# Kernel tuning notes

Measured on AMD Instinct MI355X. Metric: run time of the kernel, lower is better.

Reference implementation:

```python
import jax, jax.numpy as jnp
import numpy as np

DIM = 192
HEADS = 6
EPS = 1e-12  # torch F.normalize eps


def dwconv(x, w, b):
    # x: (B,C,H,W), w: (C,1,3,3) depthwise kernel, b: (C,)
    y = jax.lax.conv_general_dilated(
        x, w, window_strides=(1, 1), padding='SAME',
        feature_group_count=x.shape[1],
        dimension_numbers=('NCHW', 'OIHW', 'NCHW'))
    return y + b[None, :, None, None]


def setup_inputs() -> dict:
    key = jax.random.key(0)
    ks = jax.random.split(key, 9)
    x = jax.random.normal(ks[0], (8, DIM, 128, 128), dtype=jnp.float32)
    s = 1.0 / np.sqrt(9.0)
    wq = jax.random.normal(ks[1], (DIM, 1, 3, 3), dtype=jnp.float32) * s
    bq = jax.random.normal(ks[2], (DIM,), dtype=jnp.float32) * 0.01
    wk = jax.random.normal(ks[3], (DIM, 1, 3, 3), dtype=jnp.float32) * s
    bk = jax.random.normal(ks[4], (DIM,), dtype=jnp.float32) * 0.01
    wv = jax.random.normal(ks[5], (DIM, 1, 3, 3), dtype=jnp.float32) * s
    bv = jax.random.normal(ks[6], (DIM,), dtype=jnp.float32) * 0.01
    wp = jax.random.normal(ks[7], (DIM, DIM), dtype=jnp.float32) / np.sqrt(DIM)
    bp = jax.random.normal(ks[8], (DIM,), dtype=jnp.float32) * 0.01
    return {'x': x, 'wq': wq, 'bq': bq, 'wk': wk, 'bk': bk,
            'wv': wv, 'bv': bv, 'wp': wp, 'bp': bp}


def reference(x, wq, bq, wk, bk, wv, bv, wp, bp):
    b, c, h, w = x.shape
    hw = h * w
    ch = c // HEADS  # channels per head
    q = dwconv(x, wq, bq).reshape(b, HEADS, ch, hw)
    k = dwconv(x, wk, bk).reshape(b, HEADS, ch, hw)
    v = dwconv(x, wv, bv).reshape(b, HEADS, ch, hw)
    # L2 normalize along spatial dim (torch F.normalize semantics)
    q = q / jnp.maximum(jnp.linalg.norm(q, axis=-1, keepdims=True), EPS)
    k = k / jnp.maximum(jnp.linalg.norm(k, axis=-1, keepdims=True), EPS)
    attn = jnp.einsum('bhcn,bhdn->bhcd', q, k)  # (b,head,ch,ch)
    attn = jax.nn.softmax(attn, axis=-1)
    out = jnp.einsum('bhcd,bhdn->bhcn', attn, v)
    out = out.reshape(b, c, h, w)
    # 1x1 projection
    out = jnp.einsum('oc,bchw->bohw', wp, out) + bp[None, :, None, None]
    return out
```

## Files before the change

kernel.cpp:

```cpp
#include <hip/hip_runtime.h>

#define NB 8
#define NC 192
#define HEADS 6
#define CHH 32
#define IMH 128
#define IMW 128
#define NHW (IMH*IMW)
#define EPSN 1e-12f
#define NBCHW (NB*NC*NHW)

typedef __attribute__((ext_vector_type(8))) short short8_t;
typedef __attribute__((ext_vector_type(4))) float floatx4;
typedef unsigned short ushort_t;

#define MFMA_B16(a,b,c) __builtin_amdgcn_mfma_f32_16x16x32_bf16(a,b,c,0,0,0)

__device__ __forceinline__ ushort_t f2bf(float v){
  union { float f; unsigned u; } x; x.f = v;
  unsigned r = x.u + 0x7fffu + ((x.u >> 16) & 1u);
  return (ushort_t)(r >> 16);
}
__device__ __forceinline__ float bf2f(ushort_t h){
  union { unsigned u; float f; } x; x.u = ((unsigned)h) << 16;
  return x.f;
}
__device__ __forceinline__ void split8(const float* f, short8_t& hi, short8_t& lo){
#pragma unroll
  for (int i = 0; i < 8; ++i) {
    ushort_t h = f2bf(f[i]);
    hi[i] = (short)h;
    lo[i] = (short)f2bf(f[i] - bf2f(h));
  }
}

__global__ __launch_bounds__(256) void k1_conv_gram(
    const float* __restrict__ x,
    const float* __restrict__ wq, const float* __restrict__ bq,
    const float* __restrict__ wk, const float* __restrict__ bk,
    const float* __restrict__ wv, const float* __restrict__ bv,
    ushort_t* __restrict__ vhi, ushort_t* __restrict__ vlo,
    float* __restrict__ qn, float* __restrict__ kn,
    float* __restrict__ attn)
{
  __shared__ float qls[CHH*132];
  __shared__ float kls[CHH*132];
  __shared__ float vls[CHH*132];
  const int t  = threadIdx.x;
  const int b  = blockIdx.x / HEADS;
  const int h  = blockIdx.x % HEADS;
  const int r0 = blockIdx.y * 8;
  const int c   = t >> 3;
  const int s   = t & 7;
  const int px0 = s * 16;
  const int cg  = h*CHH + c;
  const float* xplane = x + (size_t)(b*NC + cg)*NHW;

  float wqr[9], wkr[9], wvr[9];
#pragma unroll
  for (int m = 0; m < 9; ++m) {
    wqr[m] = wq[cg*9+m]; wkr[m] = wk[cg*9+m]; wvr[m] = wv[cg*9+m];
  }
  const float bqv = bq[cg], bkv = bk[cg], bvv = bv[cg];

  const int lane  = t & 63;
  const int wid   = t >> 6;
  const int pw    = wid * 32;
  const int gsel  = lane >> 4;
  const int arow0 = (lane & 15)*132 + pw + gsel*8;

  floatx4 acc[2][2];
#pragma unroll
  for (int mt = 0; mt < 2; ++mt)
#pragma unroll
    for (int nt = 0; nt < 2; ++nt) acc[mt][nt] = (floatx4){0.f,0.f,0.f,0.f};
  float qnacc = 0.f, knacc = 0.f;

  for (int r = r0; r < r0 + 8; ++r) {
    float xr[3][18];
#pragma unroll
    for (int dr = 0; dr < 3; ++dr) {
      const int rr = r - 1 + dr;
      if (rr >= 0 && rr < IMH) {
        const float* rp = xplane + rr*IMW;
        xr[dr][0] = (px0 > 0) ? rp[px0-1] : 0.f;
#pragma unroll
        for (int q4 = 0; q4 < 4; ++q4) {
          const float4 fv = *(const float4*)(rp + px0 + q4*4);
          xr[dr][1+q4*4+0] = fv.x; xr[dr][1+q4*4+1] = fv.y;
          xr[dr][1+q4*4+2] = fv.z; xr[dr][1+q4*4+3] = fv.w;
        }
        xr[dr][17] = (px0 + 16 < IMW) ? rp[px0+16] : 0.f;
      } else {
#pragma unroll
        for (int j = 0; j < 18; ++j) xr[dr][j] = 0.f;
      }
    }
    float qst[4], kst[4], vst[4];
#pragma unroll
    for (int p = 0; p < 16; ++p) {
      float qa = bqv, ka = bkv, va = bvv;
#pragma unroll
      for (int dy = 0; dy < 3; ++dy)
#pragma unroll
        for (int dx = 0; dx < 3; ++dx) {
          const float xv = xr[dy][p+dx];
          qa = fmaf(wqr[dy*3+dx], xv, qa);
          ka = fmaf(wkr[dy*3+dx], xv, ka);
          va = fmaf(wvr[dy*3+dx], xv, va);
        }
      qnacc = fmaf(qa, qa, qnacc);
      knacc = fmaf(ka, ka, knacc);
      qst[p&3] = qa; kst[p&3] = ka; vst[p&3] = va;
      if ((p&3) == 3) {
        *(float4*)&qls[c*132 + px0 + p - 3] = make_float4(qst[0],qst[1],qst[2],qst[3]);
        *(float4*)&kls[c*132 + px0 + p - 3] = make_float4(kst[0],kst[1],kst[2],kst[3]);
        *(float4*)&vls[c*132 + px0 + p - 3] = make_float4(vst[0],vst[1],vst[2],vst[3]);
      }
    }
    __syncthreads();

    {
      short8_t qh[2], qlo[2], kh[2], klo[2];
#pragma unroll
      for (int mt = 0; mt < 2; ++mt) {
        float fa[8];
        const float* pq = &qls[mt*16*132 + arow0];
        float4 a0 = *(const float4*)pq; float4 a1 = *(const float4*)(pq+4);
        fa[0]=a0.x; fa[1]=a0.y; fa[2]=a0.z; fa[3]=a0.w;
        fa[4]=a1.x; fa[5]=a1.y; fa[6]=a1.z; fa[7]=a1.w;
        split8(fa, qh[mt], qlo[mt]);
        const float* pk = &kls[mt*16*132 + arow0];
        float4 b0 = *(const float4*)pk; float4 b1 = *(const float4*)(pk+4);
        fa[0]=b0.x; fa[1]=b0.y; fa[2]=b0.z; fa[3]=b0.w;
        fa[4]=b1.x; fa[5]=b1.y; fa[6]=b1.z; fa[7]=b1.w;
        split8(fa, kh[mt], klo[mt]);
      }
#pragma unroll
      for (int mt = 0; mt < 2; ++mt)
#pragma unroll
        for (int nt = 0; nt < 2; ++nt) {
          acc[mt][nt] = MFMA_B16(qh[mt],  kh[nt],  acc[mt][nt]);
          acc[mt][nt] = MFMA_B16(qh[mt],  klo[nt], acc[mt][nt]);
          acc[mt][nt] = MFMA_B16(qlo[mt], kh[nt],  acc[mt][nt]);
        }
    }

#pragma unroll
    for (int cc2 = 0; cc2 < 2; ++cc2) {
      const int id  = cc2*256 + t;
      const int oct = id & 3;
      const int px  = id >> 2;
      float f[8];
#pragma unroll
      for (int i = 0; i < 8; ++i) f[i] = vls[(oct*8+i)*132 + px];
      unsigned uh[4], ul[4];
#pragma unroll
      for (int j = 0; j < 4; ++j) {
        ushort_t h0 = f2bf(f[2*j]),   h1 = f2bf(f[2*j+1]);
        ushort_t l0 = f2bf(f[2*j]   - bf2f(h0));
        ushort_t l1 = f2bf(f[2*j+1] - bf2f(h1));
        uh[j] = (unsigned)h0 | ((unsigned)h1 << 16);
        ul[j] = (unsigned)l0 | ((unsigned)l1 << 16);
      }
      const size_t tile  = ((size_t)b*1024 + (size_t)r*8 + (px>>4))*6 + h;
      const size_t gbase = (tile*64 + (size_t)(oct*16 + (px&15))) * 8;
      *(uint4*)(vhi + gbase) = make_uint4(uh[0],uh[1],uh[2],uh[3]);
      *(uint4*)(vlo + gbase) = make_uint4(ul[0],ul[1],ul[2],ul[3]);
    }
    __syncthreads();
  }

  qnacc += __shfl_xor(qnacc, 1); qnacc += __shfl_xor(qnacc, 2); qnacc += __shfl_xor(qnacc, 4);
  knacc += __shfl_xor(knacc, 1); knacc += __shfl_xor(knacc, 2); knacc += __shfl_xor(knacc, 4);
  if (s == 0) {
    atomicAdd(qn + b*NC + cg, qnacc);
    atomicAdd(kn + b*NC + cg, knacc);
  }

  float* red = qls;
#pragma unroll
  for (int mt = 0; mt < 2; ++mt)
#pragma unroll
    for (int nt = 0; nt < 2; ++nt)
#pragma unroll
      for (int rg = 0; rg < 4; ++rg)
        red[wid*1024 + (mt*2+nt)*256 + lane*4 + rg] = acc[mt][nt][rg];
  __syncthreads();
  float* abuf = attn + (b*HEADS + h)*(CHH*CHH);
#pragma unroll
  for (int e = 0; e < 4; ++e) {
    const int idx = e*256 + t;
    const float sum = red[idx] + red[1024+idx] + red[2048+idx] + red[3072+idx];
    const int tile = idx >> 8;
    const int ln   = (idx >> 2) & 63;
    const int rg   = idx & 3;
    const int cc   = (tile>>1)*16 + (ln>>4)*4 + rg;
    const int dd   = (tile&1)*16 + (ln & 15);
    atomicAdd(abuf + cc*CHH + dd, sum);
  }
}

__global__ __launch_bounds__(256) void k2_softmax_M(
    const float* __restrict__ wp,
    const float* __restrict__ qn, const float* __restrict__ kn,
    const float* __restrict__ attn,
    short8_t* __restrict__ mhi, short8_t* __restrict__ mlo)
{
  __shared__ float a[CHH][CHH+1];
  __shared__ float qs[CHH], ks_[CHH];
  const int t = threadIdx.x;
  const int b = blockIdx.x / HEADS;
  const int h = blockIdx.x % HEADS;
  const float* raw = attn + (b*HEADS + h)*(CHH*CHH);
  if (t < CHH) {
    qs[t]  = fmaxf(sqrtf(qn[b*NC + h*CHH + t]), EPSN);
    ks_[t] = fmaxf(sqrtf(kn[b*NC + h*CHH + t]), EPSN);
  }
  __syncthreads();
#pragma unroll
  for (int rep = 0; rep < 4; ++rep) {
    const int idx = rep*256 + t;
    const int cc = idx >> 5, dd = idx & 31;
    a[cc][dd] = raw[idx] / (qs[cc] * ks_[dd]);
  }
  __syncthreads();
  if (t < CHH) {
    float m = -1e30f;
    for (int d = 0; d < CHH; ++d) m = fmaxf(m, a[t][d]);
    float sum = 0.f;
    for (int d = 0; d < CHH; ++d) { const float e = expf(a[t][d] - m); a[t][d] = e; sum += e; }
    const float inv = 1.f / sum;
    for (int d = 0; d < CHH; ++d) a[t][d] *= inv;
  }
  __syncthreads();
#pragma unroll
  for (int rep = 0; rep < 3; ++rep) {
    const int slot = rep*256 + t;
    const int o = slot >> 2;
    const int g = slot & 3;
    float m[8];
#pragma unroll
    for (int i = 0; i < 8; ++i) m[i] = 0.f;
    for (int cp = 0; cp < CHH; ++cp) {
      const float w = wp[o*NC + h*CHH + cp];
#pragma unroll
      for (int i = 0; i < 8; ++i) m[i] = fmaf(w, a[cp][g*8+i], m[i]);
    }
    short8_t hi, lo;
    split8(m, hi, lo);
    const size_t mi = (((size_t)b*12 + (o>>4))*6 + h)*64 + g*16 + (o&15);
    mhi[mi] = hi; mlo[mi] = lo;
  }
}

__global__ __launch_bounds__(256) void k3_gemm(
    const short8_t* __restrict__ vhi, const short8_t* __restrict__ vlo,
    const short8_t* __restrict__ mhi, const short8_t* __restrict__ mlo,
    const float* __restrict__ bp, float* __restrict__ out)
{
  const int t    = threadIdx.x;
  const int b    = blockIdx.y;
  const int lane = t & 63;
  const int w    = t >> 6;
  const int whw  = w & 1;
  const int wo   = w >> 1;
  const int ht0  = blockIdx.x*8 + whw*4;
  const int ot0  = wo*6;
  const int gsel = lane >> 4, l15 = lane & 15;

  floatx4 acc[6][4];
#pragma unroll
  for (int ot = 0; ot < 6; ++ot)
#pragma unroll
    for (int nt = 0; nt < 4; ++nt) acc[ot][nt] = (floatx4){0.f,0.f,0.f,0.f};

  const size_t vbase = ((size_t)b*1024 + ht0)*6;
  const size_t mbase = ((size_t)b*12 + ot0)*6;
#pragma unroll 2
  for (int ks = 0; ks < 6; ++ks) {
    short8_t bh[4], bl[4];
#pragma unroll
    for (int nt = 0; nt < 4; ++nt) {
      const size_t vi = (vbase + (size_t)nt*6 + ks)*64 + lane;
      bh[nt] = vhi[vi]; bl[nt] = vlo[vi];
    }
#pragma unroll
    for (int ot = 0; ot < 6; ++ot) {
      const size_t mi = (mbase + (size_t)ot*6 + ks)*64 + lane;
      const short8_t ah = mhi[mi];
      const short8_t al = mlo[mi];
#pragma unroll
      for (int nt = 0; nt < 4; ++nt) {
        acc[ot][nt] = MFMA_B16(ah, bh[nt], acc[ot][nt]);
        acc[ot][nt] = MFMA_B16(ah, bl[nt], acc[ot][nt]);
        acc[ot][nt] = MFMA_B16(al, bh[nt], acc[ot][nt]);
      }
    }
  }
#pragma unroll
  for (int ot = 0; ot < 6; ++ot) {
#pragma unroll
    for (int rg = 0; rg < 4; ++rg) {
      const int o = (ot0 + ot)*16 + gsel*4 + rg;
      const float bpv = bp[o];
#pragma unroll
      for (int nt = 0; nt < 4; ++nt) {
        const int hw = (ht0 + nt)*16 + l15;
        out[((size_t)(b*NC + o))*NHW + hw] = acc[ot][nt][rg] + bpv;
      }
    }
  }
}

extern "C" void kernel_launch(void* const* d_in, const int* in_sizes, int n_in,
                              void* d_out, int out_size, void* d_ws, size_t ws_size,
                              hipStream_t stream)
{
  const float* x  = (const float*)d_in[0];
  const float* wq = (const float*)d_in[1];
  const float* bq = (const float*)d_in[2];
  const float* wk = (const float*)d_in[3];
  const float* bk = (const float*)d_in[4];
  const float* wv = (const float*)d_in[5];
  const float* bv = (const float*)d_in[6];
  const float* wp = (const float*)d_in[7];
  const float* bp = (const float*)d_in[8];
  float* out = (float*)d_out;

  ushort_t* vhi = (ushort_t*)d_ws;
  ushort_t* vlo = vhi + (size_t)NBCHW;
  float* fbase  = (float*)(vlo + (size_t)NBCHW);
  float* qn     = fbase;
  float* kn     = qn + NB*NC;
  float* attn   = kn + NB*NC;
  short8_t* mhi = (short8_t*)(attn + NB*HEADS*CHH*CHH);
  short8_t* mlo = mhi + (size_t)NB*12*6*64;

  hipMemsetAsync(fbase, 0,
                 (size_t)(2*NB*NC + NB*HEADS*CHH*CHH)*sizeof(float), stream);

  k1_conv_gram<<<dim3(NB*HEADS, 16), 256, 0, stream>>>(
      x, wq, bq, wk, bk, wv, bv, vhi, vlo, qn, kn, attn);
  k2_softmax_M<<<NB*HEADS, 256, 0, stream>>>(wp, qn, kn, attn, mhi, mlo);
  k3_gemm<<<dim3(NHW/128, NB), 256, 0, stream>>>(
      (const short8_t*)vhi, (const short8_t*)vlo, mhi, mlo, bp, out);
}
```

Measured before the change: 282.2 us.

## Switch split-precision MFMA from bf16 to fp16 and store V as single fp16

Replaces the bf16 hi/lo splits with fp16 splits. V is now written as a single fp16 plane instead of hi+lo bf16, which halves V workspace traffic and cuts the final GEMM from three MFMAs per tile to two. The conv/gram kernel is restructured to process each row in two 64-pixel halves. It packs Q/K hi/lo and V as fp16 in a smaller shared buffer, with launch bounds set to target 4 blocks per SM. The risk is reduced accuracy on V from a single fp16 rounding, plus fp16 range limits on unnormalized activations.

After: 537.6 us. 90.5% more time.

```diff
diff --git a/kernel.cpp b/kernel.cpp
--- a/kernel.cpp
+++ b/kernel.cpp
@@ -10,50 +10,48 @@
 #define EPSN 1e-12f
 #define NBCHW (NB*NC*NHW)
 
-typedef __attribute__((ext_vector_type(8))) short short8_t;
+typedef _Float16 half8 __attribute__((ext_vector_type(8)));
 typedef __attribute__((ext_vector_type(4))) float floatx4;
 typedef unsigned short ushort_t;
 
-#define MFMA_B16(a,b,c) __builtin_amdgcn_mfma_f32_16x16x32_bf16(a,b,c,0,0,0)
-
-__device__ __forceinline__ ushort_t f2bf(float v){
-  union { float f; unsigned u; } x; x.f = v;
-  unsigned r = x.u + 0x7fffu + ((x.u >> 16) & 1u);
-  return (ushort_t)(r >> 16);
-}
-__device__ __forceinline__ float bf2f(ushort_t h){
-  union { unsigned u; float f; } x; x.u = ((unsigned)h) << 16;
-  return x.f;
-}
-__device__ __forceinline__ void split8(const float* f, short8_t& hi, short8_t& lo){
-#pragma unroll
-  for (int i = 0; i < 8; ++i) {
-    ushort_t h = f2bf(f[i]);
-    hi[i] = (short)h;
-    lo[i] = (short)f2bf(f[i] - bf2f(h));
-  }
-}
-
-__global__ __launch_bounds__(256) void k1_conv_gram(
+#define MFMA_F16(a,b,c) __builtin_amdgcn_mfma_f32_16x16x32_f16(a,b,c,0,0,0)
+
+__device__ __forceinline__ unsigned pk2(float a, float b){
+  union { _Float16 h[2]; unsigned u; } x;
+  x.h[0] = (_Float16)a; x.h[1] = (_Float16)b; return x.u;
+}
+__device__ __forceinline__ void pksplit(float a, float b, unsigned& hi, unsigned& lo){
+  _Float16 ha = (_Float16)a, hb = (_Float16)b;
+  float ra = a - (float)ha, rb = b - (float)hb;
+  union { _Float16 h[2]; unsigned u; } x;
+  x.h[0] = ha; x.h[1] = hb; hi = x.u;
+  x.h[0] = (_Float16)ra; x.h[1] = (_Float16)rb; lo = x.u;
+}
+
+#define PLN 1152
+#define QH 0
+#define QL (1*PLN)
+#define KH (2*PLN)
+#define KL (3*PLN)
+#define VV (4*PLN)
+
+__global__ __launch_bounds__(256, 4) void k1_conv_gram(
     const float* __restrict__ x,
     const float* __restrict__ wq, const float* __restrict__ bq,
     const float* __restrict__ wk, const float* __restrict__ bk,
     const float* __restrict__ wv, const float* __restrict__ bv,
-    ushort_t* __restrict__ vhi, ushort_t* __restrict__ vlo,
+    ushort_t* __restrict__ vout,
     float* __restrict__ qn, float* __restrict__ kn,
     float* __restrict__ attn)
 {
-  __shared__ float qls[CHH*132];
-  __shared__ float kls[CHH*132];
-  __shared__ float vls[CHH*132];
+  __shared__ unsigned sm[5*PLN];
   const int t  = threadIdx.x;
   const int b  = blockIdx.x / HEADS;
   const int h  = blockIdx.x % HEADS;
   const int r0 = blockIdx.y * 8;
-  const int c   = t >> 3;
-  const int s   = t & 7;
-  const int px0 = s * 16;
-  const int cg  = h*CHH + c;
+  const int c  = t >> 3;
+  const int s  = t & 7;
+  const int cg = h*CHH + c;
   const float* xplane = x + (size_t)(b*NC + cg)*NHW;
 
   float wqr[9], wkr[9], wvr[9];
@@ -63,11 +61,10 @@
   }
   const float bqv = bq[cg], bkv = bk[cg], bvv = bv[cg];
 
-  const int lane  = t & 63;
-  const int wid   = t >> 6;
-  const int pw    = wid * 32;
-  const int gsel  = lane >> 4;
-  const int arow0 = (lane & 15)*132 + pw + gsel*8;
+  const int lane = t & 63;
+  const int wid  = t >> 6;
+  const int gsel = lane >> 4, l15 = lane & 15;
+  const int oct  = wid;
 
   floatx4 acc[2][2];
 #pragma unroll
@@ -77,98 +74,94 @@
   float qnacc = 0.f, knacc = 0.f;
 
   for (int r = r0; r < r0 + 8; ++r) {
-    float xr[3][18];
-#pragma unroll
-    for (int dr = 0; dr < 3; ++dr) {
-      const int rr = r - 1 + dr;
-      if (rr >= 0 && rr < IMH) {
-        const float* rp = xplane + rr*IMW;
-        xr[dr][0] = (px0 > 0) ? rp[px0-1] : 0.f;
-#pragma unroll
-        for (int q4 = 0; q4 < 4; ++q4) {
-          const float4 fv = *(const float4*)(rp + px0 + q4*4);
-          xr[dr][1+q4*4+0] = fv.x; xr[dr][1+q4*4+1] = fv.y;
-          xr[dr][1+q4*4+2] = fv.z; xr[dr][1+q4*4+3] = fv.w;
+#pragma unroll
+    for (int half = 0; half < 2; ++half) {
+      const int px0 = half*64 + s*8;
+      float xr[3][10];
+#pragma unroll
+      for (int dr = 0; dr < 3; ++dr) {
+        const int rr = r - 1 + dr;
+        if (rr >= 0 && rr < IMH) {
+          const float* rp = xplane + rr*IMW;
+          xr[dr][0] = (px0 > 0) ? rp[px0-1] : 0.f;
+          const float4 f0 = *(const float4*)(rp + px0);
+          const float4 f1 = *(const float4*)(rp + px0 + 4);
+          xr[dr][1]=f0.x; xr[dr][2]=f0.y; xr[dr][3]=f0.z; xr[dr][4]=f0.w;
+          xr[dr][5]=f1.x; xr[dr][6]=f1.y; xr[dr][7]=f1.z; xr[dr][8]=f1.w;
+          xr[dr][9] = (px0 + 8 < IMW) ? rp[px0+8] : 0.f;
+        } else {
+#pragma unroll
+          for (int j = 0; j < 10; ++j) xr[dr][j] = 0.f;
         }
-        xr[dr][17] = (px0 + 16 < IMW) ? rp[px0+16] : 0.f;
-      } else {
-#pragma unroll
-        for (int j = 0; j < 18; ++j) xr[dr][j] = 0.f;
-      }
-    }
-    float qst[4], kst[4], vst[4];
-#pragma unroll
-    for (int p = 0; p < 16; ++p) {
-      float qa = bqv, ka = bkv, va = bvv;
-#pragma unroll
-      for (int dy = 0; dy < 3; ++dy)
-#pragma unroll
-        for (int dx = 0; dx < 3; ++dx) {
-          const float xv = xr[dy][p+dx];
-          qa = fmaf(wqr[dy*3+dx], xv, qa);
-          ka = fmaf(wkr[dy*3+dx], xv, ka);
-          va = fmaf(wvr[dy*3+dx], xv, va);
+      }
+      float qv[8], kv[8], vv8[8];
+#pragma unroll
+      for (int p = 0; p < 8; ++p) {
+        float qa = bqv, ka = bkv, va = bvv;
+#pragma unroll
+        for (int dy = 0; dy < 3; ++dy)
+#pragma unroll
+          for (int dx = 0; dx < 3; ++dx) {
+            const float xv = xr[dy][p+dx];
+            qa = fmaf(wqr[dy*3+dx], xv, qa);
+            ka = fmaf(wkr[dy*3+dx], xv, ka);
+            va = fmaf(wvr[dy*3+dx], xv, va);
+          }
+        qnacc = fmaf(qa, qa, qnacc);
+        knacc = fmaf(ka, ka, knacc);
+        qv[p] = qa; kv[p] = ka; vv8[p] = va;
+      }
+      unsigned qhp[4], qlp[4], khp[4], klp[4], vvp[4];
+#pragma unroll
+      for (int j = 0; j < 4; ++j) {
+        pksplit(qv[2*j], qv[2*j+1], qhp[j], qlp[j]);
+        pksplit(kv[2*j], kv[2*j+1], khp[j], klp[j]);
+        vvp[j] = pk2(vv8[2*j], vv8[2*j+1]);
+      }
+      const int wb = c*36 + s*4;
+      *(uint4*)&sm[QH + wb] = make_uint4(qhp[0],qhp[1],qhp[2],qhp[3]);
+      *(uint4*)&sm[QL + wb] = make_uint4(qlp[0],qlp[1],qlp[2],qlp[3]);
+      *(uint4*)&sm[KH + wb] = make_uint4(khp[0],khp[1],khp[2],khp[3]);
+      *(uint4*)&sm[KL + wb] = make_uint4(klp[0],klp[1],klp[2],klp[3]);
+      *(uint4*)&sm[VV + wb] = make_uint4(vvp[0],vvp[1],vvp[2],vvp[3]);
+      __syncthreads();
+
+      {
+        const int px = lane;
+        const int ph = px >> 1, sel = (px & 1) * 16;
+        unsigned w4[4];
+#pragma unroll
+        for (int i2 = 0; i2 < 4; ++i2) {
+          const unsigned ua = sm[VV + (oct*8 + 2*i2    )*36 + ph];
+          const unsigned ub = sm[VV + (oct*8 + 2*i2 + 1)*36 + ph];
+          w4[i2] = ((ua >> sel) & 0xffffu) | (((ub >> sel) & 0xffffu) << 16);
         }
-      qnacc = fmaf(qa, qa, qnacc);
-      knacc = fmaf(ka, ka, knacc);
-      qst[p&3] = qa; kst[p&3] = ka; vst[p&3] = va;
-      if ((p&3) == 3) {
-        *(float4*)&qls[c*132 + px0 + p - 3] = make_float4(qst[0],qst[1],qst[2],qst[3]);
-        *(float4*)&kls[c*132 + px0 + p - 3] = make_float4(kst[0],kst[1],kst[2],kst[3]);
-        *(float4*)&vls[c*132 + px0 + p - 3] = make_float4(vst[0],vst[1],vst[2],vst[3]);
-      }
-    }
-    __syncthreads();
-
-    {
-      short8_t qh[2], qlo[2], kh[2], klo[2];
-#pragma unroll
-      for (int mt = 0; mt < 2; ++mt) {
-        float fa[8];
-        const float* pq = &qls[mt*16*132 + arow0];
-        float4 a0 = *(const float4*)pq; float4 a1 = *(const float4*)(pq+4);
-        fa[0]=a0.x; fa[1]=a0.y; fa[2]=a0.z; fa[3]=a0.w;
-        fa[4]=a1.x; fa[5]=a1.y; fa[6]=a1.z; fa[7]=a1.w;
-        split8(fa, qh[mt], qlo[mt]);
-        const float* pk = &kls[mt*16*132 + arow0];
-        float4 b0 = *(const float4*)pk; float4 b1 = *(const float4*)(pk+4);
-        fa[0]=b0.x; fa[1]=b0.y; fa[2]=b0.z; fa[3]=b0.w;
-        fa[4]=b1.x; fa[5]=b1.y; fa[6]=b1.z; fa[7]=b1.w;
-        split8(fa, kh[mt], klo[mt]);
-      }
-#pragma unroll
-      for (int mt = 0; mt < 2; ++mt)
-#pragma unroll
-        for (int nt = 0; nt < 2; ++nt) {
-          acc[mt][nt] = MFMA_B16(qh[mt],  kh[nt],  acc[mt][nt]);
-          acc[mt][nt] = MFMA_B16(qh[mt],  klo[nt], acc[mt][nt]);
-          acc[mt][nt] = MFMA_B16(qlo[mt], kh[nt],  acc[mt][nt]);
+        const size_t tile = ((size_t)b*1024 + (size_t)r*8 + half*4 + (px>>4))*6 + h;
+        ushort_t* dst = vout + tile*512 + (size_t)(oct*16 + (px&15))*8;
+        *(uint4*)dst = make_uint4(w4[0],w4[1],w4[2],w4[3]);
+      }
+      if ((wid >> 1) == half) {
+        const int col = (wid & 1)*16 + gsel*4;
+        half8 aqh[2], aql[2], akh[2], akl[2];
+#pragma unroll
+        for (int mt = 0; mt < 2; ++mt) {
+          const int row = (mt*16 + l15)*36 + col;
+          aqh[mt] = *(const half8*)&sm[QH + row];
+          aql[mt] = *(const half8*)&sm[QL + row];
+          akh[mt] = *(const half8*)&sm[KH + row];
+          akl[mt] = *(const half8*)&sm[KL + row];
         }
-    }
-
-#pragma unroll
-    for (int cc2 = 0; cc2 < 2; ++cc2) {
-      const int id  = cc2*256 + t;
-      const int oct = id & 3;
-      const int px  = id >> 2;
-      float f[8];
-#pragma unroll
-      for (int i = 0; i < 8; ++i) f[i] = vls[(oct*8+i)*132 + px];
-      unsigned uh[4], ul[4];
-#pragma unroll
-      for (int j = 0; j < 4; ++j) {
-        ushort_t h0 = f2bf(f[2*j]),   h1 = f2bf(f[2*j+1]);
-        ushort_t l0 = f2bf(f[2*j]   - bf2f(h0));
-        ushort_t l1 = f2bf(f[2*j+1] - bf2f(h1));
-        uh[j] = (unsigned)h0 | ((unsigned)h1 << 16);
-        ul[j] = (unsigned)l0 | ((unsigned)l1 << 16);
-      }
-      const size_t tile  = ((size_t)b*1024 + (size_t)r*8 + (px>>4))*6 + h;
-      const size_t gbase = (tile*64 + (size_t)(oct*16 + (px&15))) * 8;
-      *(uint4*)(vhi + gbase) = make_uint4(uh[0],uh[1],uh[2],uh[3]);
-      *(uint4*)(vlo + gbase) = make_uint4(ul[0],ul[1],ul[2],ul[3]);
-    }
-    __syncthreads();
+#pragma unroll
+        for (int mt = 0; mt < 2; ++mt)
+#pragma unroll
+          for (int nt = 0; nt < 2; ++nt) {
+            acc[mt][nt] = MFMA_F16(aqh[mt], akh[nt], acc[mt][nt]);
+            acc[mt][nt] = MFMA_F16(aqh[mt], akl[nt], acc[mt][nt]);
+            acc[mt][nt] = MFMA_F16(aql[mt], akh[nt], acc[mt][nt]);
+          }
+      }
+      __syncthreads();
+    }
   }
 
   qnacc += __shfl_xor(qnacc, 1); qnacc += __shfl_xor(qnacc, 2); qnacc += __shfl_xor(qnacc, 4);
@@ -178,7 +171,7 @@
     atomicAdd(kn + b*NC + cg, knacc);
   }
 
-  float* red = qls;
+  float* red = (float*)sm;
 #pragma unroll
   for (int mt = 0; mt < 2; ++mt)
 #pragma unroll
@@ -205,7 +198,7 @@
     const float* __restrict__ wp,
     const float* __restrict__ qn, const float* __restrict__ kn,
     const float* __restrict__ attn,
-    short8_t* __restrict__ mhi, short8_t* __restrict__ mlo)
+    half8* __restrict__ mhi, half8* __restrict__ mlo)
 {
   __shared__ float a[CHH][CHH+1];
   __shared__ float qs[CHH], ks_[CHH];
@@ -247,16 +240,21 @@
 #pragma unroll
       for (int i = 0; i < 8; ++i) m[i] = fmaf(w, a[cp][g*8+i], m[i]);
     }
-    short8_t hi, lo;
-    split8(m, hi, lo);
+    half8 hi8, lo8;
+#pragma unroll
+    for (int i = 0; i < 8; ++i) {
+      const _Float16 hh = (_Float16)m[i];
+      hi8[i] = hh;
+      lo8[i] = (_Float16)(m[i] - (float)hh);
+    }
     const size_t mi = (((size_t)b*12 + (o>>4))*6 + h)*64 + g*16 + (o&15);
-    mhi[mi] = hi; mlo[mi] = lo;
+    mhi[mi] = hi8; mlo[mi] = lo8;
   }
 }
 
 __global__ __launch_bounds__(256) void k3_gemm(
-    const short8_t* __restrict__ vhi, const short8_t* __restrict__ vlo,
-    const short8_t* __restrict__ mhi, const short8_t* __restrict__ mlo,
+    const half8* __restrict__ v,
+    const half8* __restrict__ mhi, const half8* __restrict__ mlo,
     const float* __restrict__ bp, float* __restrict__ out)
 {
   const int t    = threadIdx.x;
@@ -277,24 +275,21 @@
 
   const size_t vbase = ((size_t)b*1024 + ht0)*6;
   const size_t mbase = ((size_t)b*12 + ot0)*6;
-#pragma unroll 2
+#pragma unroll
   for (int ks = 0; ks < 6; ++ks) {
-    short8_t bh[4], bl[4];
-#pragma unroll
-    for (int nt = 0; nt < 4; ++nt) {
-      const size_t vi = (vbase + (size_t)nt*6 + ks)*64 + lane;
-      bh[nt] = vhi[vi]; bl[nt] = vlo[vi];
-    }
+    half8 bf[4];
+#pragma unroll
+    for (int nt = 0; nt < 4; ++nt)
+      bf[nt] = v[(vbase + (size_t)nt*6 + ks)*64 + lane];
 #pragma unroll
     for (int ot = 0; ot < 6; ++ot) {
       const size_t mi = (mbase + (size_t)ot*6 + ks)*64 + lane;
-      const short8_t ah = mhi[mi];
-      const short8_t al = mlo[mi];
+      const half8 ah = mhi[mi];
+      const half8 al = mlo[mi];
 #pragma unroll
       for (int nt = 0; nt < 4; ++nt) {
-        acc[ot][nt] = MFMA_B16(ah, bh[nt], acc[ot][nt]);
-        acc[ot][nt] = MFMA_B16(ah, bl[nt], acc[ot][nt]);
-        acc[ot][nt] = MFMA_B16(al, bh[nt], acc[ot][nt]);
+        acc[ot][nt] = MFMA_F16(ah, bf[nt], acc[ot][nt]);
+        acc[ot][nt] = MFMA_F16(al, bf[nt], acc[ot][nt]);
       }
     }
   }
@@ -328,21 +323,20 @@
   const float* bp = (const float*)d_in[8];
   float* out = (float*)d_out;
 
-  ushort_t* vhi = (ushort_t*)d_ws;
-  ushort_t* vlo = vhi + (size_t)NBCHW;
-  float* fbase  = (float*)(vlo + (size_t)NBCHW);
-  float* qn     = fbase;
-  float* kn     = qn + NB*NC;
-  float* attn   = kn + NB*NC;
-  short8_t* mhi = (short8_t*)(attn + NB*HEADS*CHH*CHH);
-  short8_t* mlo = mhi + (size_t)NB*12*6*64;
+  ushort_t* vout = (ushort_t*)d_ws;
+  float* fbase   = (float*)(vout + (size_t)NBCHW);
+  float* qn      = fbase;
+  float* kn      = qn + NB*NC;
+  float* attn    = kn + NB*NC;
+  half8* mhi     = (half8*)(attn + NB*HEADS*CHH*CHH);
+  half8* mlo     = mhi + (size_t)NB*12*6*64;
 
   hipMemsetAsync(fbase, 0,
                  (size_t)(2*NB*NC + NB*HEADS*CHH*CHH)*sizeof(float), stream);
 
   k1_conv_gram<<<dim3(NB*HEADS, 16), 256, 0, stream>>>(
-      x, wq, bq, wk, bk, wv, bv, vhi, vlo, qn, kn, attn);
+      x, wq, bq, wk, bk, wv, bv, vout, qn, kn, attn);
   k2_softmax_M<<<NB*HEADS, 256, 0, stream>>>(wp, qn, kn, attn, mhi, mlo);
   k3_gemm<<<dim3(NHW/128, NB), 256, 0, stream>>>(
-      (const short8_t*)vhi, (const short8_t*)vlo, mhi, mlo, bp, out);
-}
+      (const half8*)vout, mhi, mlo, bp, out);
+}
```
